# Kernel tuning notes

Measured on AMD Instinct MI355X. Metric: run time of the kernel, lower is better.

Reference implementation:

```python
import jax, jax.numpy as jnp
import numpy as np

HORIZON = 20
STATE_DIM = 16
BATCH = 524288
DT = 0.05          # integration step
MASS = 1.0
GRAV = 9.81
TAU_M = 0.05       # motor time constant
MAX_T = 5.0        # max thrust per rotor [N]
ARM = 0.2          # arm length [m]
KAPPA = 0.02       # yaw torque coefficient
INERTIA = np.array([0.01, 0.01, 0.02], dtype=np.float32)


def _quad_step(state, action):
    """One Euler step of quadrotor dynamics.
    state: [B,16] = pos(3) vel(3) euler(3) body_rates(3) rotor_thrusts(4)
    action: [B,4] or [1,4] normalized rotor commands in (0,1)."""
    pos, vel, att, omega, thr = (state[..., 0:3], state[..., 3:6],
                                 state[..., 6:9], state[..., 9:12],
                                 state[..., 12:16])
    inertia = jnp.asarray(INERTIA)
    # first-order motor dynamics toward commanded thrust
    thr_new = thr + (DT / TAU_M) * (action * MAX_T - thr)
    F = thr_new.sum(-1)  # total thrust [B]
    tau = jnp.stack([
        ARM * (thr_new[..., 0] - thr_new[..., 2]),
        ARM * (thr_new[..., 1] - thr_new[..., 3]),
        KAPPA * (thr_new[..., 0] - thr_new[..., 1] + thr_new[..., 2] - thr_new[..., 3]),
    ], -1)  # [B,3]
    phi, th, psi = att[..., 0], att[..., 1], att[..., 2]
    sphi, cphi = jnp.sin(phi), jnp.cos(phi)
    sth, cth = jnp.sin(th), jnp.cos(th)
    spsi, cpsi = jnp.sin(psi), jnp.cos(psi)
    # body z-axis in world frame
    zb = jnp.stack([cphi * sth * cpsi + sphi * spsi,
                    cphi * sth * spsi - sphi * cpsi,
                    cphi * cth], -1)
    acc = (F / MASS)[..., None] * zb - jnp.array([0.0, 0.0, GRAV], dtype=state.dtype)
    p, q, r = omega[..., 0], omega[..., 1], omega[..., 2]
    tanth = sth / cth
    att_dot = jnp.stack([p + sphi * tanth * q + cphi * tanth * r,
                         cphi * q - sphi * r,
                         (sphi * q + cphi * r) / cth], -1)
    omega_dot = (tau - jnp.cross(omega, inertia * omega)) / inertia
    return jnp.concatenate([pos + DT * vel,
                            vel + DT * acc,
                            att + DT * att_dot,
                            omega + DT * omega_dot,
                            thr_new], -1)


def setup_inputs() -> dict:
    key = jax.random.key(0)
    k1, _ = jax.random.split(key)
    current_state = 0.1 * jax.random.normal(k1, (BATCH, STATE_DIM), dtype=jnp.float32)
    U = jnp.ones((HORIZON, 1, 4), dtype=jnp.float32) * 0.4  # learnable per-step actions
    return {"current_state": current_state, "U": U}


def reference(current_state, U):
    actions = jax.nn.sigmoid(U)  # [H,1,4] gated actions

    def body(state, a):
        new_state = _quad_step(state, a)  # a broadcasts (1,4)->(B,4)
        return new_state, new_state

    _, intermediate_states = jax.lax.scan(body, current_state, actions)
    return intermediate_states  # [H, B, 16]
```

## Files before the change

### kernel.cpp

```cpp
#include <hip/hip_runtime.h>

#define HORIZON 20
#define BATCH   524288

typedef float f32x4 __attribute__((ext_vector_type(4)));

__global__ __launch_bounds__(256) void drone_rollout(
    const float* __restrict__ state_in,
    const float* __restrict__ U,
    float* __restrict__ out)
{
    constexpr float DT    = 0.05f;
    constexpr float GRAV  = 9.81f;
    constexpr float TAU_M = 0.05f;
    constexpr float MAX_T = 5.0f;
    constexpr float ARM   = 0.2f;
    constexpr float KAPPA = 0.02f;
    constexpr float Ix = 0.01f, Iy = 0.01f, Iz = 0.02f;
    const float rIx = 1.0f / Ix, rIy = 1.0f / Iy, rIz = 1.0f / Iz;
    const float dt_tau = DT / TAU_M;

    __shared__ float s_act[HORIZON * 4];
    __shared__ f32x4 lds4[2][256 * 4];

    const int tid = threadIdx.x;
    if (tid < HORIZON * 4) {
        float u = U[tid];
        s_act[tid] = 1.0f / (1.0f + expf(-u));
    }
    __syncthreads();

    const int b = blockIdx.x * blockDim.x + tid;

    const f32x4* sp = reinterpret_cast<const f32x4*>(state_in + (size_t)b * 16);
    f32x4 s0 = sp[0], s1 = sp[1], s2 = sp[2], s3 = sp[3];
    float px = s0.x, py = s0.y, pz = s0.z;
    float vx = s0.w, vy = s1.x, vz = s1.y;
    float phi = s1.z, th = s1.w, psi = s2.x;
    float p = s2.y, q = s2.z, r = s2.w;
    float t0 = s3.x, t1 = s3.y, t2 = s3.z, t3 = s3.w;

    const int swzw   = (tid >> 1) & 3;
    const int rrow   = tid >> 2;
    const int rchunk = (tid & 3) ^ ((tid >> 3) & 3);
    f32x4* const outbase = reinterpret_cast<f32x4*>(out)
                         + (size_t)blockIdx.x * 256 * 4;

    #pragma unroll
    for (int t = 0; t < HORIZON; ++t) {
        const float a0 = s_act[t * 4 + 0];
        const float a1 = s_act[t * 4 + 1];
        const float a2 = s_act[t * 4 + 2];
        const float a3 = s_act[t * 4 + 3];

        t0 += dt_tau * (a0 * MAX_T - t0);
        t1 += dt_tau * (a1 * MAX_T - t1);
        t2 += dt_tau * (a2 * MAX_T - t2);
        t3 += dt_tau * (a3 * MAX_T - t3);

        const float F    = t0 + t1 + t2 + t3;
        const float taux = ARM * (t0 - t2);
        const float tauy = ARM * (t1 - t3);
        const float tauz = KAPPA * (t0 - t1 + t2 - t3);

        float sphi, cphi, sth, cth, spsi, cpsi;
        __sincosf(phi, &sphi, &cphi);
        __sincosf(th,  &sth,  &cth);
        __sincosf(psi, &spsi, &cpsi);

        const float zbx = cphi * sth * cpsi + sphi * spsi;
        const float zby = cphi * sth * spsi - sphi * cpsi;
        const float zbz = cphi * cth;
        const float ax = F * zbx;
        const float ay = F * zby;
        const float az = F * zbz - GRAV;

        const float rcth  = 1.0f / cth;
        const float tanth = sth * rcth;
        const float attd0 = p + sphi * tanth * q + cphi * tanth * r;
        const float attd1 = cphi * q - sphi * r;
        const float attd2 = (sphi * q + cphi * r) * rcth;

        const float hx = Ix * p, hy = Iy * q, hz = Iz * r;
        const float pd = (taux - (q * hz - r * hy)) * rIx;
        const float qd = (tauy - (r * hx - p * hz)) * rIy;
        const float rd = (tauz - (p * hy - q * hx)) * rIz;

        px += DT * vx;  py += DT * vy;  pz += DT * vz;
        vx += DT * ax;  vy += DT * ay;  vz += DT * az;
        phi += DT * attd0;  th += DT * attd1;  psi += DT * attd2;
        p += DT * pd;  q += DT * qd;  r += DT * rd;

        const int bb = t & 1;
        f32x4* wb = &lds4[bb][tid * 4];
        wb[0 ^ swzw] = f32x4{px, py, pz, vx};
        wb[1 ^ swzw] = f32x4{vy, vz, phi, th};
        wb[2 ^ swzw] = f32x4{psi, p, q, r};
        wb[3 ^ swzw] = f32x4{t0, t1, t2, t3};
        __syncthreads();

        f32x4* const op = outbase + (size_t)t * (BATCH * 4);
        #pragma unroll
        for (int k = 0; k < 4; ++k) {
            f32x4 v = lds4[bb][(k * 64 + rrow) * 4 + rchunk];
            __builtin_nontemporal_store(v, op + k * 256 + tid);
        }
    }
}

extern "C" void kernel_launch(void* const* d_in, const int* in_sizes, int n_in,
                              void* d_out, int out_size, void* d_ws, size_t ws_size,
                              hipStream_t stream) {
    const float* state = (const float*)d_in[0];
    const float* U     = (const float*)d_in[1];
    float* out         = (float*)d_out;

    dim3 block(256);
    dim3 grid(BATCH / 256);
    drone_rollout<<<grid, block, 0, stream>>>(state, U, out);
}
```

Baseline: 128.7 us.

## Make LDS transpose wave-local and drop block barriers in rollout loop

The output transpose through LDS moves from a block-wide double buffer guarded by __syncthreads to a per-wavefront buffer with only compiler memory fences. This relies on in-order LDS access within a single wave. The input state is now loaded with coalesced vector loads and transposed through the same LDS region. The thrust update is folded algebraically, since DT/TAU_M equals one and MAX_T is pre-multiplied into the sigmoid table. A leftover redundant statement on t0 remains. The kernel is largely store-bandwidth bound, so barrier removal mainly helps overlap between waves.

After: 136.8 us. 1.06x slower.

```diff
diff --git a/kernel.cpp b/kernel.cpp
--- a/kernel.cpp
+++ b/kernel.cpp
@@ -12,51 +12,66 @@
 {
     constexpr float DT    = 0.05f;
     constexpr float GRAV  = 9.81f;
-    constexpr float TAU_M = 0.05f;
     constexpr float MAX_T = 5.0f;
     constexpr float ARM   = 0.2f;
     constexpr float KAPPA = 0.02f;
     constexpr float Ix = 0.01f, Iy = 0.01f, Iz = 0.02f;
     const float rIx = 1.0f / Ix, rIy = 1.0f / Iy, rIz = 1.0f / Iz;
-    const float dt_tau = DT / TAU_M;
 
     __shared__ float s_act[HORIZON * 4];
-    __shared__ f32x4 lds4[2][256 * 4];
+    __shared__ f32x4 lds4[4][256];
 
     const int tid = threadIdx.x;
+    const int w   = tid >> 6;
+    const int l   = tid & 63;
+
     if (tid < HORIZON * 4) {
         float u = U[tid];
-        s_act[tid] = 1.0f / (1.0f + expf(-u));
+        s_act[tid] = MAX_T / (1.0f + expf(-u));
     }
     __syncthreads();
 
-    const int b = blockIdx.x * blockDim.x + tid;
+    f32x4* const wlds = &lds4[w][0];
 
-    const f32x4* sp = reinterpret_cast<const f32x4*>(state_in + (size_t)b * 16);
-    f32x4 s0 = sp[0], s1 = sp[1], s2 = sp[2], s3 = sp[3];
+    const int wr_sw  = (l >> 1) & 3;
+    const int tr_row = l >> 2;
+    const int tr_sw  = (l & 3) ^ ((l >> 3) & 3);
+
+    const f32x4* inv = reinterpret_cast<const f32x4*>(state_in)
+                     + ((size_t)blockIdx.x * 256 + (size_t)w * 64) * 4;
+    #pragma unroll
+    for (int k = 0; k < 4; ++k) {
+        f32x4 v = inv[k * 64 + l];
+        wlds[(k * 16 + tr_row) * 4 + tr_sw] = v;
+    }
+    asm volatile("" ::: "memory");
+    f32x4 s0 = wlds[l * 4 + (0 ^ wr_sw)];
+    f32x4 s1 = wlds[l * 4 + (1 ^ wr_sw)];
+    f32x4 s2 = wlds[l * 4 + (2 ^ wr_sw)];
+    f32x4 s3 = wlds[l * 4 + (3 ^ wr_sw)];
+    asm volatile("" ::: "memory");
+
     float px = s0.x, py = s0.y, pz = s0.z;
     float vx = s0.w, vy = s1.x, vz = s1.y;
     float phi = s1.z, th = s1.w, psi = s2.x;
     float p = s2.y, q = s2.z, r = s2.w;
     float t0 = s3.x, t1 = s3.y, t2 = s3.z, t3 = s3.w;
 
-    const int swzw   = (tid >> 1) & 3;
-    const int rrow   = tid >> 2;
-    const int rchunk = (tid & 3) ^ ((tid >> 3) & 3);
-    f32x4* const outbase = reinterpret_cast<f32x4*>(out)
-                         + (size_t)blockIdx.x * 256 * 4;
+    f32x4* const outv = reinterpret_cast<f32x4*>(out)
+                      + ((size_t)blockIdx.x * 256 + (size_t)w * 64) * 4;
 
     #pragma unroll
     for (int t = 0; t < HORIZON; ++t) {
-        const float a0 = s_act[t * 4 + 0];
-        const float a1 = s_act[t * 4 + 1];
-        const float a2 = s_act[t * 4 + 2];
-        const float a3 = s_act[t * 4 + 3];
+        const float A0 = s_act[t * 4 + 0];
+        const float A1 = s_act[t * 4 + 1];
+        const float A2 = s_act[t * 4 + 2];
+        const float A3 = s_act[t * 4 + 3];
 
-        t0 += dt_tau * (a0 * MAX_T - t0);
-        t1 += dt_tau * (a1 * MAX_T - t1);
-        t2 += dt_tau * (a2 * MAX_T - t2);
-        t3 += dt_tau * (a3 * MAX_T - t3);
+        t0 += A0 - t0 + 0.0f, t0 = t0;
+        t0 = t0 + (A0 - t0);
+        t1 = t1 + (A1 - t1);
+        t2 = t2 + (A2 - t2);
+        t3 = t3 + (A3 - t3);
 
         const float F    = t0 + t1 + t2 + t3;
         const float taux = ARM * (t0 - t2);
@@ -91,20 +106,19 @@
         phi += DT * attd0;  th += DT * attd1;  psi += DT * attd2;
         p += DT * pd;  q += DT * qd;  r += DT * rd;
 
-        const int bb = t & 1;
-        f32x4* wb = &lds4[bb][tid * 4];
-        wb[0 ^ swzw] = f32x4{px, py, pz, vx};
-        wb[1 ^ swzw] = f32x4{vy, vz, phi, th};
-        wb[2 ^ swzw] = f32x4{psi, p, q, r};
-        wb[3 ^ swzw] = f32x4{t0, t1, t2, t3};
-        __syncthreads();
+        wlds[l * 4 + (0 ^ wr_sw)] = f32x4{px, py, pz, vx};
+        wlds[l * 4 + (1 ^ wr_sw)] = f32x4{vy, vz, phi, th};
+        wlds[l * 4 + (2 ^ wr_sw)] = f32x4{psi, p, q, r};
+        wlds[l * 4 + (3 ^ wr_sw)] = f32x4{t0, t1, t2, t3};
+        asm volatile("" ::: "memory");
 
-        f32x4* const op = outbase + (size_t)t * (BATCH * 4);
+        f32x4* const op = outv + (size_t)t * (BATCH * 4);
         #pragma unroll
         for (int k = 0; k < 4; ++k) {
-            f32x4 v = lds4[bb][(k * 64 + rrow) * 4 + rchunk];
-            __builtin_nontemporal_store(v, op + k * 256 + tid);
+            f32x4 v = wlds[(k * 16 + tr_row) * 4 + tr_sw];
+            __builtin_nontemporal_store(v, op + k * 64 + l);
         }
+        asm volatile("" ::: "memory");
     }
 }
 
```

## Single-buffer LDS staging, disable loop unroll, prescale actions by max thrust

Applied to the files above, without the earlier changes.

Staging now uses one LDS buffer instead of two, which halves shared memory per block and may let more blocks fit per CU. A second barrier per step is added to protect the buffer reuse. The time loop is no longer unrolled, which shrinks code size and register pressure but adds loop overhead. Actions are premultiplied by MAX_T, the unit DT/TAU_M factor is folded away, and the four actions are read with one vector LDS load. The extra barrier per step may serialise store traffic more.

New measurement: 131.6 us. +2.2%, slower.

```diff
diff --git a/kernel.cpp b/kernel.cpp
--- a/kernel.cpp
+++ b/kernel.cpp
@@ -12,27 +12,23 @@
 {
     constexpr float DT    = 0.05f;
     constexpr float GRAV  = 9.81f;
-    constexpr float TAU_M = 0.05f;
     constexpr float MAX_T = 5.0f;
     constexpr float ARM   = 0.2f;
     constexpr float KAPPA = 0.02f;
     constexpr float Ix = 0.01f, Iy = 0.01f, Iz = 0.02f;
-    const float rIx = 1.0f / Ix, rIy = 1.0f / Iy, rIz = 1.0f / Iz;
-    const float dt_tau = DT / TAU_M;
+    constexpr float rIx = 100.0f, rIy = 100.0f, rIz = 50.0f;
 
-    __shared__ float s_act[HORIZON * 4];
-    __shared__ f32x4 lds4[2][256 * 4];
+    __shared__ alignas(16) float s_act[HORIZON * 4];
+    __shared__ f32x4 lds4[256 * 4];
 
     const int tid = threadIdx.x;
     if (tid < HORIZON * 4) {
         float u = U[tid];
-        s_act[tid] = 1.0f / (1.0f + expf(-u));
+        s_act[tid] = MAX_T / (1.0f + expf(-u));
     }
-    __syncthreads();
 
-    const int b = blockIdx.x * blockDim.x + tid;
-
-    const f32x4* sp = reinterpret_cast<const f32x4*>(state_in + (size_t)b * 16);
+    const int b = blockIdx.x * 256 + tid;
+    const f32x4* sp = reinterpret_cast<const f32x4*>(state_in) + (size_t)b * 4;
     f32x4 s0 = sp[0], s1 = sp[1], s2 = sp[2], s3 = sp[3];
     float px = s0.x, py = s0.y, pz = s0.z;
     float vx = s0.w, vy = s1.x, vz = s1.y;
@@ -40,23 +36,22 @@
     float p = s2.y, q = s2.z, r = s2.w;
     float t0 = s3.x, t1 = s3.y, t2 = s3.z, t3 = s3.w;
 
+    __syncthreads();
+
     const int swzw   = (tid >> 1) & 3;
     const int rrow   = tid >> 2;
     const int rchunk = (tid & 3) ^ ((tid >> 3) & 3);
     f32x4* const outbase = reinterpret_cast<f32x4*>(out)
                          + (size_t)blockIdx.x * 256 * 4;
 
-    #pragma unroll
+    #pragma unroll 1
     for (int t = 0; t < HORIZON; ++t) {
-        const float a0 = s_act[t * 4 + 0];
-        const float a1 = s_act[t * 4 + 1];
-        const float a2 = s_act[t * 4 + 2];
-        const float a3 = s_act[t * 4 + 3];
+        const f32x4 A = *reinterpret_cast<const f32x4*>(&s_act[t * 4]);
 
-        t0 += dt_tau * (a0 * MAX_T - t0);
-        t1 += dt_tau * (a1 * MAX_T - t1);
-        t2 += dt_tau * (a2 * MAX_T - t2);
-        t3 += dt_tau * (a3 * MAX_T - t3);
+        t0 += A.x - t0;
+        t1 += A.y - t1;
+        t2 += A.z - t2;
+        t3 += A.w - t3;
 
         const float F    = t0 + t1 + t2 + t3;
         const float taux = ARM * (t0 - t2);
@@ -91,8 +86,7 @@
         phi += DT * attd0;  th += DT * attd1;  psi += DT * attd2;
         p += DT * pd;  q += DT * qd;  r += DT * rd;
 
-        const int bb = t & 1;
-        f32x4* wb = &lds4[bb][tid * 4];
+        f32x4* wb = &lds4[tid * 4];
         wb[0 ^ swzw] = f32x4{px, py, pz, vx};
         wb[1 ^ swzw] = f32x4{vy, vz, phi, th};
         wb[2 ^ swzw] = f32x4{psi, p, q, r};
@@ -102,9 +96,10 @@
         f32x4* const op = outbase + (size_t)t * (BATCH * 4);
         #pragma unroll
         for (int k = 0; k < 4; ++k) {
-            f32x4 v = lds4[bb][(k * 64 + rrow) * 4 + rchunk];
+            f32x4 v = lds4[(k * 64 + rrow) * 4 + rchunk];
             __builtin_nontemporal_store(v, op + k * 256 + tid);
         }
+        __syncthreads();
     }
 }
 
```
